# Optimization experiments

Measured on AMD Instinct MI355X. Metric: run time of the kernel, lower is better.

Reference implementation:

```python
import jax, jax.numpy as jnp
import numpy as np

B, N, F_IN, H_DIM, HEADS, DH, LAYERS, OUT, BS = 8192, 64, 12, 64, 4, 16, 3, 128, 8
LN_EPS = 1e-5


def _build_adj():
    # 8-neighbor grid adjacency + self loops, as in _register_adjacency
    adj = np.zeros((N, N), np.float32)
    for i in range(N):
        r, c = divmod(i, BS)
        for dr in (-1, 0, 1):
            for dc in (-1, 0, 1):
                if dr == 0 and dc == 0:
                    continue
            
                nr, nc = r + dr, c + dc
                if 0 <= nr < BS and 0 <= nc < BS:
                    adj[i, nr * BS + nc] = 1.0
    adj += np.eye(N, dtype=np.float32)
    return (adj > 0).astype(np.int32)


def setup_inputs() -> dict:
    key = jax.random.key(0)
    ks = jax.random.split(key, 16)
    s = 0.05
    return {
        "x": jax.random.normal(ks[0], (B, N, F_IN), jnp.float32),
        "adj": jnp.asarray(_build_adj()),
        "W_in": jax.random.normal(ks[1], (F_IN, H_DIM), jnp.float32) * s,
        "b_in": jnp.zeros((H_DIM,), jnp.float32),
        "Wq": jax.random.normal(ks[2], (LAYERS, H_DIM, H_DIM), jnp.float32) * s,
        "Wk": jax.random.normal(ks[3], (LAYERS, H_DIM, H_DIM), jnp.float32) * s,
        "Wv": jax.random.normal(ks[4], (LAYERS, H_DIM, H_DIM), jnp.float32) * s,
        "Wo": jax.random.normal(ks[5], (LAYERS, H_DIM, H_DIM), jnp.float32) * s,
        "bo": jnp.zeros((LAYERS, H_DIM), jnp.float32),
        "ln_g": jnp.ones((LAYERS, H_DIM), jnp.float32),
        "ln_b": jnp.zeros((LAYERS, H_DIM), jnp.float32),
        "Wp1": jax.random.normal(ks[6], (H_DIM, H_DIM), jnp.float32) * s,
        "bp1": jnp.zeros((H_DIM,), jnp.float32),
        "Wp2": jax.random.normal(ks[7], (H_DIM, OUT), jnp.float32) * s,
        "bp2": jnp.zeros((OUT,), jnp.float32),
    }


def _layer_norm(h, g, b):
    mu = jnp.mean(h, axis=-1, keepdims=True)
    var = jnp.mean(jnp.square(h - mu), axis=-1, keepdims=True)
    return (h - mu) * jax.lax.rsqrt(var + LN_EPS) * g + b


def reference(x, adj, W_in, b_in, Wq, Wk, Wv, Wo, bo, ln_g, ln_b, Wp1, bp1, Wp2, bp2):
    b, n = x.shape[:2]
    mask = (adj == 0)[None, None]          # (1,1,N,N)
    scale = 1.0 / jnp.sqrt(jnp.float32(DH))
    h = x @ W_in + b_in                    # (B,N,H_DIM)
    for l in range(LAYERS):
        q = (h @ Wq[l]).reshape(b, n, HEADS, DH)
        k = (h @ Wk[l]).reshape(b, n, HEADS, DH)
        v = (h @ Wv[l]).reshape(b, n, HEADS, DH)
        scores = jnp.einsum('bihd,bjhd->bhij', q, k) * scale   # (B,H,N,N)
        scores = jnp.where(mask, -jnp.inf, scores)
        attn = jax.nn.softmax(scores, axis=-1)                 # dropout = identity (eval)
        o = jnp.einsum('bhij,bjhd->bihd', attn, v).reshape(b, n, HEADS * DH)
        o = o @ Wo[l] + bo[l]
        h = _layer_norm(h + o, ln_g[l], ln_b[l])
    pooled = h.mean(axis=1)                                    # (B,H_DIM)
    return jax.nn.relu(pooled @ Wp1 + bp1) @ Wp2 + bp2         # (B,OUT)
```

## Files before the change

kernel.cpp:

```cpp
#include <hip/hip_runtime.h>
#include <stdint.h>

#define NB       64
#define FIN      12
#define HD       64
#define NHEADS   4
#define DHEAD    16
#define NLAYERS  3
#define ODIM     128
#define LN_EPS   1e-5f
#define BTOT     8192

#define NTH      256
#define NWAVE    4
#define NW       (NLAYERS * 4)
#define WFRAG    4096
#define WIN_U16  2048
#define NTILES   10
#define MSK_U32  (NTILES * 64 * 2)

#define HROW     72

typedef unsigned int       u32;
typedef unsigned short     u16;
typedef unsigned long long u64;
typedef _Float16           f16;

typedef f16    f16x8 __attribute__((ext_vector_type(8)));
typedef f16    f16x4 __attribute__((ext_vector_type(4)));
typedef f16    h2    __attribute__((ext_vector_type(2)));
typedef __fp16 hh2   __attribute__((ext_vector_type(2)));
typedef float  f32x4 __attribute__((ext_vector_type(4)));
union U128h { uint4 u; f16x8 v8; f16x4 v4h[2]; h2 v2[4]; };
union U64h  { uint2 u; f16x4 v4; h2 h[2]; u32 w[2]; u16 s[4]; };

#if __has_builtin(__builtin_amdgcn_exp2f)
  __device__ __forceinline__ float e2(float x) { return __builtin_amdgcn_exp2f(x); }
#else
  __device__ __forceinline__ float e2(float x) { return exp2f(x); }
#endif

__device__ __forceinline__ float fdot2h(h2 a, h2 b, float c) {
#if __has_builtin(__builtin_amdgcn_fdot2)
  return __builtin_amdgcn_fdot2(a, b, c, false);
#else
  return c + (float)a[0] * (float)b[0] + (float)a[1] * (float)b[1];
#endif
}

#if __has_builtin(__builtin_amdgcn_cvt_pkrtz)
__device__ __forceinline__ u32 packh2(float a, float b) {
  hh2 p = __builtin_amdgcn_cvt_pkrtz(a, b);
  return *(u32*)&p;
}
#else
__device__ __forceinline__ u32 packh2(float a, float b) {
  h2 p = {(f16)a, (f16)b};
  return *(u32*)&p;
}
#endif

#if __has_builtin(__builtin_amdgcn_mfma_f32_16x16x16f16)
__device__ __forceinline__ f32x4 mfma16(f16x4 a, f16x4 b, f32x4 c) {
  return __builtin_amdgcn_mfma_f32_16x16x16f16(a, b, c, 0, 0, 0);
}
#elif __has_builtin(__builtin_amdgcn_mfma_f32_16x16x16_f16)
__device__ __forceinline__ f32x4 mfma16(f16x4 a, f16x4 b, f32x4 c) {
  return __builtin_amdgcn_mfma_f32_16x16x16_f16(a, b, c, 0, 0, 0);
}
#else
__device__ __forceinline__ f32x4 mfma16(f16x4 a, f16x4 b, f32x4 c) {
  f16x8 a8 = {a[0], a[1], a[2], a[3], (f16)0, (f16)0, (f16)0, (f16)0};
  f16x8 b8 = {b[0], b[1], b[2], b[3], (f16)0, (f16)0, (f16)0, (f16)0};
  return __builtin_amdgcn_mfma_f32_16x16x32_f16(a8, b8, c, 0, 0, 0);
}
#endif

__device__ __forceinline__ f32x4 mfma32(f16x8 a, f16x8 b, f32x4 c) {
  return __builtin_amdgcn_mfma_f32_16x16x32_f16(a, b, c, 0, 0, 0);
}

__device__ __forceinline__ f16x4 pa4(u32 w0, u32 w1) {
  U64h u; u.w[0] = w0; u.w[1] = w1; return u.v4;
}

struct __align__(16) Smem {
  u32   Msk[MSK_U32];
  float scr[NWAVE][128];
  u16   hob[NWAVE][64 * HROW];
};

extern "C" __global__ void __launch_bounds__(256)
prep_pack(const float* __restrict__ Wq, const float* __restrict__ Wk,
          const float* __restrict__ Wv, const float* __restrict__ Wo,
          const float* __restrict__ W_in, const int* __restrict__ adj,
          u16* __restrict__ wsW) {
  const int w = blockIdx.x;
  if (w < NW) {
    const int l = w >> 2, ty = w & 3;
    u16* dst = wsW + w * WFRAG;
    if (ty == 2) {
      const float* src = Wv + l * HD * HD;
      for (int f = threadIdx.x; f < 512; f += 256) {
        const int lane = f & 63, fi = f >> 6;
        const int dt = fi >> 1, c = fi & 1;
        const int mm = lane & 15, mq = (lane >> 4) & 3;
        u16 tmp[8];
        #pragma unroll
        for (int e = 0; e < 8; ++e) {
          const int kk = c * 2 + (e >> 2), j = e & 3;
          f16 hv = (f16)src[(kk * 16 + mq * 4 + j) * HD + dt * 16 + mm];
          tmp[e] = *(u16*)&hv;
        }
        *(uint4*)(dst + f * 8) = *(const uint4*)tmp;
      }
    } else {
      const float* src = (ty == 0 ? Wq : ty == 1 ? Wk : Wo) + l * HD * HD;
      const float sc = (ty == 0) ? (0.25f * 1.44269504f) : 1.0f;
      for (int f = threadIdx.x; f < 512; f += 256) {
        const int lane = f & 63, kh = (f >> 6) & 1, nt = f >> 7;
        const int n  = nt * 16 + (lane & 15);
        const int k0 = kh * 32 + ((lane >> 4) & 3) * 8;
        u16 tmp[8];
        #pragma unroll
        for (int j = 0; j < 8; ++j) {
          f16 hv = (f16)(src[(k0 + j) * HD + n] * sc);
          tmp[j] = *(u16*)&hv;
        }
        *(uint4*)(dst + f * 8) = *(const uint4*)tmp;
      }
    }
  } else if (w == NW) {
    const int t = threadIdx.x;
    const int mt = t >> 6, lane = t & 63;
    const int mm = lane & 15, qq = (lane >> 4) & 3;
    u16 tmp[8];
    #pragma unroll
    for (int j = 0; j < 8; ++j) {
      const int k = qq * 8 + j;
      f16 hv = (k < FIN) ? (f16)W_in[k * HD + mt * 16 + mm] : (f16)0.0f;
      tmp[j] = *(u16*)&hv;
    }
    *(uint4*)(wsW + NW * WFRAG + t * 8) = *(const uint4*)tmp;
  } else {
    static const int TIv[NTILES] = {0, 0, 1, 1, 1, 2, 2, 2, 3, 3};
    static const int TJv[NTILES] = {0, 1, 0, 1, 2, 1, 2, 3, 2, 3};
    u32* wsMsk = (u32*)(wsW + NW * WFRAG + WIN_U16);
    for (int idx = threadIdx.x; idx < MSK_U32; idx += 256) {
      const int tile = idx >> 7, rem = idx & 127;
      const int l = rem >> 1, pr = rem & 1;
      const int i  = TIv[tile] * 16 + (l & 15);
      const int j0 = TJv[tile] * 16 + ((l >> 4) & 3) * 4 + pr * 2;
      const u32 lo = (adj[i * NB + j0]     != 0) ? 0x3C00u : 0u;
      const u32 hi = (adj[i * NB + j0 + 1] != 0) ? 0x3C00u : 0u;
      wsMsk[idx] = lo | (hi << 16);
    }
  }
}

extern "C" __global__ void __launch_bounds__(NTH, 2)
gnn_fused(const float* __restrict__ x, const float* __restrict__ b_in,
          const u16* __restrict__ wsW, const float* __restrict__ bo,
          const float* __restrict__ ln_g, const float* __restrict__ ln_b,
          const float* __restrict__ Wp1, const float* __restrict__ bp1,
          const float* __restrict__ Wp2, const float* __restrict__ bp2,
          float* __restrict__ out) {
  __shared__ Smem s;
  const int tb = threadIdx.x;
  const int t  = tb & 63;
  const int wv = tb >> 6;
  const int m  = t & 15, q = t >> 4;
  const int g  = (int)blockIdx.x * NWAVE + wv;

  const u16* wsWin = wsW + NW * WFRAG;
  u16* hw = s.hob[wv];

  {
    const uint4* mg4 = (const uint4*)(wsWin + WIN_U16);
    if (tb < 256) ((uint4*)s.Msk)[tb] = mg4[tb];
    if (tb < 64)  ((uint4*)s.Msk)[256 + tb] = mg4[256 + tb];
  }
  __syncthreads();

  f32x4 hr[4][4];
  {
    #pragma unroll
    for (int ng = 0; ng < 4; ++ng) {
      U128h xb;
      xb.u = make_uint4(0u, 0u, 0u, 0u);
      const float* gx = x + (size_t)(g * NB + ng * 16 + m) * FIN;
      if (q == 0) {
        const float4 fa = *(const float4*)gx;
        const float4 fb = *(const float4*)(gx + 4);
        xb.u = make_uint4(packh2(fa.x, fa.y), packh2(fa.z, fa.w),
                          packh2(fb.x, fb.y), packh2(fb.z, fb.w));
      } else if (q == 1) {
        const float4 fc = *(const float4*)(gx + 8);
        xb.u.x = packh2(fc.x, fc.y);
        xb.u.y = packh2(fc.z, fc.w);
      }
      #pragma unroll
      for (int mt = 0; mt < 4; ++mt) {
        U128h aw;
        aw.u = *(const uint4*)(wsWin + (mt * 64 + t) * 8);
        f32x4 acc = {0.f, 0.f, 0.f, 0.f};
        acc = mfma32(aw.v8, xb.v8, acc);
        const f32x4 b4 = *(const f32x4*)&b_in[mt * 16 + q * 4];
        hr[ng][mt] = acc + b4;
      }
    }
  }

  #pragma unroll 1
  for (int l = 0; l < NLAYERS; ++l) {
    const u16* wq  = wsW + (l * 4 + 0) * WFRAG;
    const u16* wk  = wsW + (l * 4 + 1) * WFRAG;
    const u16* wvd = wsW + (l * 4 + 2) * WFRAG;
    const u16* wo  = wsW + (l * 4 + 3) * WFRAG;
    const f32x4 z4 = {0.f, 0.f, 0.f, 0.f};

    U128h aV[8], aQ[8];
    #pragma unroll
    for (int i = 0; i < 8; ++i) aV[i].u = *(const uint4*)(wvd + (i * 64 + t) * 8);
    #pragma unroll
    for (int i = 0; i < 8; ++i) aQ[i].u = *(const uint4*)(wq + (i * 64 + t) * 8);

    u32 hp[4][8];
    #pragma unroll
    for (int ng = 0; ng < 4; ++ng)
      #pragma unroll
      for (int mt = 0; mt < 4; ++mt) {
        hp[ng][2 * mt]     = packh2(hr[ng][mt][0], hr[ng][mt][1]);
        hp[ng][2 * mt + 1] = packh2(hr[ng][mt][2], hr[ng][mt][3]);
      }

    #pragma unroll
    for (int ng = 0; ng < 4; ++ng)
      #pragma unroll
      for (int mt = 0; mt < 4; ++mt)
        *(uint2*)&hw[(ng * 16 + m) * HROW + mt * 16 + q * 4] =
            make_uint2(hp[ng][2 * mt], hp[ng][2 * mt + 1]);

    U64h vf[4][4];
    #pragma unroll
    for (int dt = 0; dt < 4; ++dt) {
      #pragma unroll
      for (int nt = 0; nt < 4; ++nt) {
        f32x4 acc = z4;
        acc = mfma16(pa4(hp[nt][0], hp[nt][1]), aV[dt * 2].v4h[0], acc);
        acc = mfma16(pa4(hp[nt][2], hp[nt][3]), aV[dt * 2].v4h[1], acc);
        acc = mfma16(pa4(hp[nt][4], hp[nt][5]), aV[dt * 2 + 1].v4h[0], acc);
        acc = mfma16(pa4(hp[nt][6], hp[nt][7]), aV[dt * 2 + 1].v4h[1], acc);
        vf[dt][nt].w[0] = packh2(acc[0], acc[1]);
        vf[dt][nt].w[1] = packh2(acc[2], acc[3]);
      }
    }
    U128h aK[8];
    #pragma unroll
    for (int i = 0; i < 8; ++i) aK[i].u = *(const uint4*)(wk + (i * 64 + t) * 8);

    U64h qf[4][4];
    #pragma unroll
    for (int ng = 0; ng < 4; ++ng) {
      U128h b0, b1;
      b0.u = *(const uint4*)&hw[(ng * 16 + m) * HROW + q * 8];
      b1.u = *(const uint4*)&hw[(ng * 16 + m) * HROW + 32 + q * 8];
      #pragma unroll
      for (int mt = 0; mt < 4; ++mt) {
        f32x4 acc = z4;
        acc = mfma32(aQ[mt * 2].v8,     b0.v8, acc);
        acc = mfma32(aQ[mt * 2 + 1].v8, b1.v8, acc);
        qf[mt][ng].w[0] = packh2(acc[0], acc[1]);
        qf[mt][ng].w[1] = packh2(acc[2], acc[3]);
      }
    }
    U64h kf[4][4];
    #pragma unroll
    for (int ng = 0; ng < 4; ++ng) {
      U128h b0, b1;
      b0.u = *(const uint4*)&hw[(ng * 16 + m) * HROW + q * 8];
      b1.u = *(const uint4*)&hw[(ng * 16 + m) * HROW + 32 + q * 8];
      #pragma unroll
      for (int mt = 0; mt < 4; ++mt) {
        f32x4 acc = z4;
        acc = mfma32(aK[mt * 2].v8,     b0.v8, acc);
        acc = mfma32(aK[mt * 2 + 1].v8, b1.v8, acc);
        kf[mt][ng].w[0] = packh2(acc[0], acc[1]);
        kf[mt][ng].w[1] = packh2(acc[2], acc[3]);
      }
    }

    u32 opk[4][8];
    {
      const h2 one2 = {(f16)1.0f, (f16)1.0f};
#define ATTN_HT(HH, TI, TJ0, NTJ, T0)                                          \
      {                                                                        \
        f32x4 ot = z4;                                                         \
        float dsum = 0.0f;                                                     \
        _Pragma("unroll")                                                      \
        for (int dt = 0; dt < (NTJ); ++dt) {                                   \
          const int tj = (TJ0) + dt;                                           \
          f32x4 st = mfma16(kf[HH][tj].v4, qf[HH][TI].v4, z4);                 \
          const uint2 mmv = *(const uint2*)&s.Msk[((T0) + dt) * 128 + (t << 1)]; \
          U64h pp;                                                             \
          pp.w[0] = packh2(e2(st[0]), e2(st[1]));                              \
          pp.w[1] = packh2(e2(st[2]), e2(st[3]));                              \
          pp.h[0] *= *(const h2*)&mmv.x;                                       \
          pp.h[1] *= *(const h2*)&mmv.y;                                       \
          dsum = fdot2h(pp.h[0], one2, dsum);                                  \
          dsum = fdot2h(pp.h[1], one2, dsum);                                  \
          ot = mfma16(vf[HH][tj].v4, pp.v4, ot);                               \
        }                                                                      \
        dsum += __shfl_xor(dsum, 16, 64);                                      \
        dsum += __shfl_xor(dsum, 32, 64);                                      \
        const float rinv = 1.0f / dsum;                                        \
        opk[TI][2 * (HH)]     = packh2(ot[0] * rinv, ot[1] * rinv);            \
        opk[TI][2 * (HH) + 1] = packh2(ot[2] * rinv, ot[3] * rinv);            \
      }
      #pragma unroll
      for (int hh = 0; hh < 4; ++hh) {
        ATTN_HT(hh, 0, 0, 2, 0)
        ATTN_HT(hh, 1, 0, 3, 2)
        ATTN_HT(hh, 2, 1, 3, 5)
        ATTN_HT(hh, 3, 2, 2, 8)
      }
#undef ATTN_HT
    }

    U128h aO[8];
    #pragma unroll
    for (int i = 0; i < 8; ++i) aO[i].u = *(const uint4*)(wo + (i * 64 + t) * 8);

    #pragma unroll
    for (int ti = 0; ti < 4; ++ti)
      #pragma unroll
      for (int hh = 0; hh < 4; ++hh)
        *(uint2*)&hw[(ti * 16 + m) * HROW + hh * 16 + q * 4] =
            make_uint2(opk[ti][2 * hh], opk[ti][2 * hh + 1]);

    {
      #pragma unroll
      for (int ng = 0; ng < 4; ++ng) {
        U128h ob0, ob1;
        ob0.u = *(const uint4*)&hw[(ng * 16 + m) * HROW + q * 8];
        ob1.u = *(const uint4*)&hw[(ng * 16 + m) * HROW + 32 + q * 8];
        float s1 = 0.0f, s2 = 0.0f;
        #pragma unroll
        for (int mt = 0; mt < 4; ++mt) {
          f32x4 acc = z4;
          acc = mfma32(aO[mt * 2].v8,     ob0.v8, acc);
          acc = mfma32(aO[mt * 2 + 1].v8, ob1.v8, acc);
          const f32x4 bo4 = *(const f32x4*)&bo[l * HD + mt * 16 + q * 4];
          const f32x4 u4 = hr[ng][mt] + acc + bo4;
          hr[ng][mt] = u4;
          #pragma unroll
          for (int r = 0; r < 4; ++r) { s1 += u4[r]; s2 += u4[r] * u4[r]; }
        }
        s1 += __shfl_xor(s1, 16, 64); s1 += __shfl_xor(s1, 32, 64);
        s2 += __shfl_xor(s2, 16, 64); s2 += __shfl_xor(s2, 32, 64);
        const float mu  = s1 * (1.0f / 64.0f);
        const float var = s2 * (1.0f / 64.0f) - mu * mu;
        const float rs  = rsqrtf(var + LN_EPS);
        #pragma unroll
        for (int mt = 0; mt < 4; ++mt) {
          const f32x4 g4  = *(const f32x4*)&ln_g[l * HD + mt * 16 + q * 4];
          const f32x4 be4 = *(const f32x4*)&ln_b[l * HD + mt * 16 + q * 4];
          #pragma unroll
          for (int r = 0; r < 4; ++r)
            hr[ng][mt][r] = (hr[ng][mt][r] - mu) * rs * g4[r] + be4[r];
        }
      }
    }
  }

  {
    #pragma unroll
    for (int mt = 0; mt < 4; ++mt) {
      f32x4 v = hr[0][mt] + hr[1][mt] + hr[2][mt] + hr[3][mt];
      #pragma unroll
      for (int r = 0; r < 4; ++r) {
        float vv = v[r];
        vv += __shfl_xor(vv, 1, 64); vv += __shfl_xor(vv, 2, 64);
        vv += __shfl_xor(vv, 4, 64); vv += __shfl_xor(vv, 8, 64);
        v[r] = vv * (1.0f / 64.0f);
      }
      if (m == 0) *(f32x4*)&s.scr[wv][mt * 16 + q * 4] = v;
    }
  }
  {
    float acc = bp1[t];
    #pragma unroll 8
    for (int k = 0; k < HD; ++k) acc = fmaf(s.scr[wv][k], Wp1[k * HD + t], acc);
    s.scr[wv][64 + t] = fmaxf(acc, 0.0f);
  }
  {
    float a0 = bp2[t], a1 = bp2[t + 64];
    #pragma unroll 8
    for (int c = 0; c < HD; ++c) {
      const float yc = s.scr[wv][64 + c];
      a0 = fmaf(yc, Wp2[c * ODIM + t], a0);
      a1 = fmaf(yc, Wp2[c * ODIM + t + 64], a1);
    }
    out[g * ODIM + t]      = a0;
    out[g * ODIM + t + 64] = a1;
  }
}

extern "C" void kernel_launch(void* const* d_in, const int* in_sizes, int n_in,
                              void* d_out, int out_size, void* d_ws, size_t ws_size,
                              hipStream_t stream) {
  const float* x    = (const float*)d_in[0];
  const int*   adj  = (const int*)d_in[1];
  const float* W_in = (const float*)d_in[2];
  const float* b_in = (const float*)d_in[3];
  const float* Wq   = (const float*)d_in[4];
  const float* Wk   = (const float*)d_in[5];
  const float* Wv   = (const float*)d_in[6];
  const float* Wo   = (const float*)d_in[7];
  const float* bo   = (const float*)d_in[8];
  const float* lng  = (const float*)d_in[9];
  const float* lnb  = (const float*)d_in[10];
  const float* Wp1  = (const float*)d_in[11];
  const float* bp1  = (const float*)d_in[12];
  const float* Wp2  = (const float*)d_in[13];
  const float* bp2  = (const float*)d_in[14];
  float* outp = (float*)d_out;
  u16*   wsW  = (u16*)d_ws;

  hipLaunchKernelGGL(prep_pack, dim3(NW + 2), dim3(256), 0, stream,
                     Wq, Wk, Wv, Wo, W_in, adj, wsW);
  hipLaunchKernelGGL(gnn_fused, dim3(BTOT / NWAVE), dim3(NTH), 0, stream,
                     x, b_in, wsW, bo, lng, lnb, Wp1, bp1, Wp2, bp2, outp);
}
```

Before: 229.7 us.

## Split each graph across two waves with LDS exchange of boundary K/V tiles

Each graph is now processed by a pair of waves, each owning 32 of the 64 nodes, instead of one wave per graph. The adjacent boundary K/V tile is exchanged through shared memory with block barriers, and the pooling and MLP head are split across the pair. This halves per-wave register state (hr, fragments) and doubles the wave count to raise occupancy and parallelism. In exchange it adds two block-wide barriers per layer, redundant weight-fragment loads per wave, and more total blocks.

```diff
diff --git a/kernel.cpp b/kernel.cpp
--- a/kernel.cpp
+++ b/kernel.cpp
@@ -18,7 +18,6 @@
 #define WIN_U16  2048
 #define NTILES   10
 #define MSK_U32  (NTILES * 64 * 2)
-
 #define HROW     72
 
 typedef unsigned int       u32;
@@ -86,9 +85,12 @@
 
 struct __align__(16) Smem {
   u32   Msk[MSK_U32];
-  float scr[NWAVE][128];
-  u16   hob[NWAVE][64 * HROW];
+  uint2 xK[2 * 2 * 4 * 64];
+  uint2 xV[2 * 2 * 4 * 64];
+  u16   hob[NWAVE][32 * HROW];
 };
+
+#define XIDX(P, H, HH, T) ((((P) * 2 + (H)) * 4 + (HH)) * 64 + (T))
 
 extern "C" __global__ void __launch_bounds__(256)
 prep_pack(const float* __restrict__ Wq, const float* __restrict__ Wk,
@@ -166,11 +168,13 @@
           const float* __restrict__ Wp2, const float* __restrict__ bp2,
           float* __restrict__ out) {
   __shared__ Smem s;
-  const int tb = threadIdx.x;
-  const int t  = tb & 63;
-  const int wv = tb >> 6;
-  const int m  = t & 15, q = t >> 4;
-  const int g  = (int)blockIdx.x * NWAVE + wv;
+  const int tb   = threadIdx.x;
+  const int t    = tb & 63;
+  const int wv   = tb >> 6;
+  const int p    = wv >> 1;
+  const int half = wv & 1;
+  const int m    = t & 15, q = t >> 4;
+  const int g    = (int)blockIdx.x * 2 + p;
 
   const u16* wsWin = wsW + NW * WFRAG;
   u16* hw = s.hob[wv];
@@ -182,10 +186,11 @@
   }
   __syncthreads();
 
-  f32x4 hr[4][4];
+  f32x4 hr[2][4];
   {
     #pragma unroll
-    for (int ng = 0; ng < 4; ++ng) {
+    for (int ngl = 0; ngl < 2; ++ngl) {
+      const int ng = 2 * half + ngl;
       U128h xb;
       xb.u = make_uint4(0u, 0u, 0u, 0u);
       const float* gx = x + (size_t)(g * NB + ng * 16 + m) * FIN;
@@ -206,7 +211,7 @@
         f32x4 acc = {0.f, 0.f, 0.f, 0.f};
         acc = mfma32(aw.v8, xb.v8, acc);
         const f32x4 b4 = *(const f32x4*)&b_in[mt * 16 + q * 4];
-        hr[ng][mt] = acc + b4;
+        hr[ngl][mt] = acc + b4;
       }
     }
   }
@@ -225,83 +230,91 @@
     #pragma unroll
     for (int i = 0; i < 8; ++i) aQ[i].u = *(const uint4*)(wq + (i * 64 + t) * 8);
 
-    u32 hp[4][8];
-    #pragma unroll
-    for (int ng = 0; ng < 4; ++ng)
+    u32 hp[2][8];
+    #pragma unroll
+    for (int ngl = 0; ngl < 2; ++ngl)
       #pragma unroll
       for (int mt = 0; mt < 4; ++mt) {
-        hp[ng][2 * mt]     = packh2(hr[ng][mt][0], hr[ng][mt][1]);
-        hp[ng][2 * mt + 1] = packh2(hr[ng][mt][2], hr[ng][mt][3]);
-      }
-
-    #pragma unroll
-    for (int ng = 0; ng < 4; ++ng)
+        hp[ngl][2 * mt]     = packh2(hr[ngl][mt][0], hr[ngl][mt][1]);
+        hp[ngl][2 * mt + 1] = packh2(hr[ngl][mt][2], hr[ngl][mt][3]);
+      }
+    #pragma unroll
+    for (int ngl = 0; ngl < 2; ++ngl)
       #pragma unroll
       for (int mt = 0; mt < 4; ++mt)
-        *(uint2*)&hw[(ng * 16 + m) * HROW + mt * 16 + q * 4] =
-            make_uint2(hp[ng][2 * mt], hp[ng][2 * mt + 1]);
-
-    U64h vf[4][4];
+        *(uint2*)&hw[(ngl * 16 + m) * HROW + mt * 16 + q * 4] =
+            make_uint2(hp[ngl][2 * mt], hp[ngl][2 * mt + 1]);
+
+    U64h vo[4][2];
     #pragma unroll
     for (int dt = 0; dt < 4; ++dt) {
       #pragma unroll
-      for (int nt = 0; nt < 4; ++nt) {
+      for (int ntl = 0; ntl < 2; ++ntl) {
         f32x4 acc = z4;
-        acc = mfma16(pa4(hp[nt][0], hp[nt][1]), aV[dt * 2].v4h[0], acc);
-        acc = mfma16(pa4(hp[nt][2], hp[nt][3]), aV[dt * 2].v4h[1], acc);
-        acc = mfma16(pa4(hp[nt][4], hp[nt][5]), aV[dt * 2 + 1].v4h[0], acc);
-        acc = mfma16(pa4(hp[nt][6], hp[nt][7]), aV[dt * 2 + 1].v4h[1], acc);
-        vf[dt][nt].w[0] = packh2(acc[0], acc[1]);
-        vf[dt][nt].w[1] = packh2(acc[2], acc[3]);
+        acc = mfma16(pa4(hp[ntl][0], hp[ntl][1]), aV[dt * 2].v4h[0], acc);
+        acc = mfma16(pa4(hp[ntl][2], hp[ntl][3]), aV[dt * 2].v4h[1], acc);
+        acc = mfma16(pa4(hp[ntl][4], hp[ntl][5]), aV[dt * 2 + 1].v4h[0], acc);
+        acc = mfma16(pa4(hp[ntl][6], hp[ntl][7]), aV[dt * 2 + 1].v4h[1], acc);
+        vo[dt][ntl].w[0] = packh2(acc[0], acc[1]);
+        vo[dt][ntl].w[1] = packh2(acc[2], acc[3]);
       }
     }
     U128h aK[8];
     #pragma unroll
     for (int i = 0; i < 8; ++i) aK[i].u = *(const uint4*)(wk + (i * 64 + t) * 8);
 
-    U64h qf[4][4];
-    #pragma unroll
-    for (int ng = 0; ng < 4; ++ng) {
+    U64h qf[4][2], ko[4][2];
+    #pragma unroll
+    for (int ngl = 0; ngl < 2; ++ngl) {
       U128h b0, b1;
-      b0.u = *(const uint4*)&hw[(ng * 16 + m) * HROW + q * 8];
-      b1.u = *(const uint4*)&hw[(ng * 16 + m) * HROW + 32 + q * 8];
+      b0.u = *(const uint4*)&hw[(ngl * 16 + m) * HROW + q * 8];
+      b1.u = *(const uint4*)&hw[(ngl * 16 + m) * HROW + 32 + q * 8];
       #pragma unroll
       for (int mt = 0; mt < 4; ++mt) {
         f32x4 acc = z4;
         acc = mfma32(aQ[mt * 2].v8,     b0.v8, acc);
         acc = mfma32(aQ[mt * 2 + 1].v8, b1.v8, acc);
-        qf[mt][ng].w[0] = packh2(acc[0], acc[1]);
-        qf[mt][ng].w[1] = packh2(acc[2], acc[3]);
-      }
-    }
-    U64h kf[4][4];
-    #pragma unroll
-    for (int ng = 0; ng < 4; ++ng) {
-      U128h b0, b1;
-      b0.u = *(const uint4*)&hw[(ng * 16 + m) * HROW + q * 8];
-      b1.u = *(const uint4*)&hw[(ng * 16 + m) * HROW + 32 + q * 8];
+        qf[mt][ngl].w[0] = packh2(acc[0], acc[1]);
+        qf[mt][ngl].w[1] = packh2(acc[2], acc[3]);
+      }
       #pragma unroll
       for (int mt = 0; mt < 4; ++mt) {
         f32x4 acc = z4;
         acc = mfma32(aK[mt * 2].v8,     b0.v8, acc);
         acc = mfma32(aK[mt * 2 + 1].v8, b1.v8, acc);
-        kf[mt][ng].w[0] = packh2(acc[0], acc[1]);
-        kf[mt][ng].w[1] = packh2(acc[2], acc[3]);
-      }
-    }
-
-    u32 opk[4][8];
-    {
-      const h2 one2 = {(f16)1.0f, (f16)1.0f};
-#define ATTN_HT(HH, TI, TJ0, NTJ, T0)                                          \
-      {                                                                        \
-        f32x4 ot = z4;                                                         \
-        float dsum = 0.0f;                                                     \
-        _Pragma("unroll")                                                      \
-        for (int dt = 0; dt < (NTJ); ++dt) {                                   \
-          const int tj = (TJ0) + dt;                                           \
-          f32x4 st = mfma16(kf[HH][tj].v4, qf[HH][TI].v4, z4);                 \
-          const uint2 mmv = *(const uint2*)&s.Msk[((T0) + dt) * 128 + (t << 1)]; \
+        ko[mt][ngl].w[0] = packh2(acc[0], acc[1]);
+        ko[mt][ngl].w[1] = packh2(acc[2], acc[3]);
+      }
+    }
+
+    if (half == 0) {
+      #pragma unroll
+      for (int hh = 0; hh < 4; ++hh) {
+        s.xK[XIDX(p, 0, hh, t)] = ko[hh][1].u;
+        s.xV[XIDX(p, 0, hh, t)] = vo[hh][1].u;
+      }
+    } else {
+      #pragma unroll
+      for (int hh = 0; hh < 4; ++hh) {
+        s.xK[XIDX(p, 1, hh, t)] = ko[hh][0].u;
+        s.xV[XIDX(p, 1, hh, t)] = vo[hh][0].u;
+      }
+    }
+    __syncthreads();
+    U64h kf_f[4], vf_f[4];
+    #pragma unroll
+    for (int hh = 0; hh < 4; ++hh) {
+      kf_f[hh].u = s.xK[XIDX(p, half ^ 1, hh, t)];
+      vf_f[hh].u = s.xV[XIDX(p, half ^ 1, hh, t)];
+    }
+    __syncthreads();
+
+    u32 opk[2][8];
+    const h2 one2 = {(f16)1.0f, (f16)1.0f};
+#define ATTN_STEP(KF, VF, MT)                                                  \
+        {                                                                      \
+          f32x4 st = mfma16((KF).v4, qv, z4);                                  \
+          const uint2 mmv = *(const uint2*)&s.Msk[(MT) * 128 + (t << 1)];      \
           U64h pp;                                                             \
           pp.w[0] = packh2(e2(st[0]), e2(st[1]));                              \
           pp.w[1] = packh2(e2(st[2]), e2(st[3]));                              \
@@ -309,41 +322,73 @@
           pp.h[1] *= *(const h2*)&mmv.y;                                       \
           dsum = fdot2h(pp.h[0], one2, dsum);                                  \
           dsum = fdot2h(pp.h[1], one2, dsum);                                  \
-          ot = mfma16(vf[HH][tj].v4, pp.v4, ot);                               \
-        }                                                                      \
+          ot = mfma16((VF).v4, pp.v4, ot);                                     \
+        }
+#define ATTN_FIN(TIL, HH)                                                      \
         dsum += __shfl_xor(dsum, 16, 64);                                      \
         dsum += __shfl_xor(dsum, 32, 64);                                      \
         const float rinv = 1.0f / dsum;                                        \
-        opk[TI][2 * (HH)]     = packh2(ot[0] * rinv, ot[1] * rinv);            \
-        opk[TI][2 * (HH) + 1] = packh2(ot[2] * rinv, ot[3] * rinv);            \
-      }
+        opk[TIL][2 * (HH)]     = packh2(ot[0] * rinv, ot[1] * rinv);           \
+        opk[TIL][2 * (HH) + 1] = packh2(ot[2] * rinv, ot[3] * rinv);
+    if (half == 0) {
       #pragma unroll
       for (int hh = 0; hh < 4; ++hh) {
-        ATTN_HT(hh, 0, 0, 2, 0)
-        ATTN_HT(hh, 1, 0, 3, 2)
-        ATTN_HT(hh, 2, 1, 3, 5)
-        ATTN_HT(hh, 3, 2, 2, 8)
-      }
-#undef ATTN_HT
-    }
+        {
+          const f16x4 qv = qf[hh][0].v4;
+          f32x4 ot = z4; float dsum = 0.0f;
+          ATTN_STEP(ko[hh][0], vo[hh][0], 0)
+          ATTN_STEP(ko[hh][1], vo[hh][1], 1)
+          ATTN_FIN(0, hh)
+        }
+        {
+          const f16x4 qv = qf[hh][1].v4;
+          f32x4 ot = z4; float dsum = 0.0f;
+          ATTN_STEP(ko[hh][0], vo[hh][0], 2)
+          ATTN_STEP(ko[hh][1], vo[hh][1], 3)
+          ATTN_STEP(kf_f[hh],  vf_f[hh],  4)
+          ATTN_FIN(1, hh)
+        }
+      }
+    } else {
+      #pragma unroll
+      for (int hh = 0; hh < 4; ++hh) {
+        {
+          const f16x4 qv = qf[hh][0].v4;
+          f32x4 ot = z4; float dsum = 0.0f;
+          ATTN_STEP(kf_f[hh],  vf_f[hh],  5)
+          ATTN_STEP(ko[hh][0], vo[hh][0], 6)
+          ATTN_STEP(ko[hh][1], vo[hh][1], 7)
+          ATTN_FIN(0, hh)
+        }
+        {
+          const f16x4 qv = qf[hh][1].v4;
+          f32x4 ot = z4; float dsum = 0.0f;
+          ATTN_STEP(ko[hh][0], vo[hh][0], 8)
+          ATTN_STEP(ko[hh][1], vo[hh][1], 9)
+          ATTN_FIN(1, hh)
+        }
+      }
+    }
+#undef ATTN_STEP
+#undef ATTN_FIN
 
     U128h aO[8];
     #pragma unroll
     for (int i = 0; i < 8; ++i) aO[i].u = *(const uint4*)(wo + (i * 64 + t) * 8);
 
     #pragma unroll
-    for (int ti = 0; ti < 4; ++ti)
+    for (int til = 0; til < 2; ++til)
       #pragma unroll
       for (int hh = 0; hh < 4; ++hh)
-        *(uint2*)&hw[(ti * 16 + m) * HROW + hh * 16 + q * 4] =
-            make_uint2(opk[ti][2 * hh], opk[ti][2 * hh + 1]);
+        *(uint2*)&hw[(til * 16 + m) * HROW + hh * 16 + q * 4] =
+            make_uint2(opk[til][2 * hh], opk[til][2 * hh + 1]);
 
     {
       #pragma unroll
-      for (int ng = 0; ng < 4; ++ng) {
+      for (int ngl = 0; ngl < 2; ++ngl) {
         U128h ob0, ob1;
-        ob0.u = *(const uint4*)&hw[(ng * 16 + m) * HROW + q * 8];
-        ob1.u = *(const uint4*)&hw[(ng * 16 + m) * HROW + 32 + q * 8];
+        ob0.u = *(const uint4*)&hw[(ngl * 16 + m) * HROW + q * 8];
+        ob1.u = *(const uint4*)&hw[(ngl * 16 + m) * HROW + 32 + q * 8];
         float s1 = 0.0f, s2 = 0.0f;
         #pragma unroll
         for (int mt = 0; mt < 4; ++mt) {
@@ -351,8 +396,8 @@
           acc = mfma32(aO[mt * 2].v8,     ob0.v8, acc);
           acc = mfma32(aO[mt * 2 + 1].v8, ob1.v8, acc);
           const f32x4 bo4 = *(const f32x4*)&bo[l * HD + mt * 16 + q * 4];
-          const f32x4 u4 = hr[ng][mt] + acc + bo4;
-          hr[ng][mt] = u4;
+          const f32x4 u4 = hr[ngl][mt] + acc + bo4;
+          hr[ngl][mt] = u4;
           #pragma unroll
           for (int r = 0; r < 4; ++r) { s1 += u4[r]; s2 += u4[r] * u4[r]; }
         }
@@ -367,16 +412,18 @@
           const f32x4 be4 = *(const f32x4*)&ln_b[l * HD + mt * 16 + q * 4];
           #pragma unroll
           for (int r = 0; r < 4; ++r)
-            hr[ng][mt][r] = (hr[ng][mt][r] - mu) * rs * g4[r] + be4[r];
-        }
-      }
-    }
-  }
-
+            hr[ngl][mt][r] = (hr[ngl][mt][r] - mu) * rs * g4[r] + be4[r];
+        }
+      }
+    }
+  }
+
+  float* scrP = (float*)s.xV;
+  float* scrY = (float*)hw;
   {
     #pragma unroll
     for (int mt = 0; mt < 4; ++mt) {
-      f32x4 v = hr[0][mt] + hr[1][mt] + hr[2][mt] + hr[3][mt];
+      f32x4 v = hr[0][mt] + hr[1][mt];
       #pragma unroll
       for (int r = 0; r < 4; ++r) {
         float vv = v[r];
@@ -384,25 +431,24 @@
         vv += __shfl_xor(vv, 4, 64); vv += __shfl_xor(vv, 8, 64);
         v[r] = vv * (1.0f / 64.0f);
       }
-      if (m == 0) *(f32x4*)&s.scr[wv][mt * 16 + q * 4] = v;
-    }
-  }
+      if (m == 0) *(f32x4*)&scrP[(p * 2 + half) * 64 + mt * 16 + q * 4] = v;
+    }
+  }
+  __syncthreads();
   {
+    const float* pa = &scrP[(p * 2) * 64];
+    const float* pb = &scrP[(p * 2 + 1) * 64];
     float acc = bp1[t];
     #pragma unroll 8
-    for (int k = 0; k < HD; ++k) acc = fmaf(s.scr[wv][k], Wp1[k * HD + t], acc);
-    s.scr[wv][64 + t] = fmaxf(acc, 0.0f);
+    for (int k = 0; k < HD; ++k) acc = fmaf(pa[k] + pb[k], Wp1[k * HD + t], acc);
+    scrY[t] = fmaxf(acc, 0.0f);
   }
   {
-    float a0 = bp2[t], a1 = bp2[t + 64];
+    const int c = half * 64 + t;
+    float a0 = bp2[c];
     #pragma unroll 8
-    for (int c = 0; c < HD; ++c) {
-      const float yc = s.scr[wv][64 + c];
-      a0 = fmaf(yc, Wp2[c * ODIM + t], a0);
-      a1 = fmaf(yc, Wp2[c * ODIM + t + 64], a1);
-    }
-    out[g * ODIM + t]      = a0;
-    out[g * ODIM + t + 64] = a1;
+    for (int k = 0; k < HD; ++k) a0 = fmaf(scrY[k], Wp2[k * ODIM + c], a0);
+    out[g * ODIM + c] = a0;
   }
 }
 
@@ -429,6 +475,6 @@
 
   hipLaunchKernelGGL(prep_pack, dim3(NW + 2), dim3(256), 0, stream,
                      Wq, Wk, Wv, Wo, W_in, adj, wsW);
-  hipLaunchKernelGGL(gnn_fused, dim3(BTOT / NWAVE), dim3(NTH), 0, stream,
+  hipLaunchKernelGGL(gnn_fused, dim3(BTOT / 2), dim3(NTH), 0, stream,
                      x, b_in, wsW, bo, lng, lnb, Wp1, bp1, Wp2, bp2, outp);
 }
```

New measurement: 255.5 us. +11.2%, slower.
